# Performance work log

Measured on AMD Instinct MI355X. Metric: run time of the kernel, lower is better.

Reference implementation:

```python
import jax, jax.numpy as jnp
import numpy as np

DIM, N_HEAD, N_KV, HEAD_DIM = 4096, 32, 8, 128
B, S = 2, 2048


def apply_rotary_emb(x, freqs_cis):
    # x: [B, S, H, D]; freqs_cis: [S, D//2, 2]
    xs = x.reshape(x.shape[:-1] + (-1, 2))            # [B,S,H,D/2,2]
    f = freqs_cis.reshape(1, xs.shape[1], 1, xs.shape[3], 2)
    x0, x1 = xs[..., 0], xs[..., 1]
    f0, f1 = f[..., 0], f[..., 1]
    out = jnp.stack([x0 * f0 - x1 * f1, x0 * f1 + x1 * f0], axis=-1)
    return out.reshape(x.shape).astype(x.dtype)


def setup_inputs() -> dict:
    key = jax.random.key(0)
    k1, k2, k3, k4 = jax.random.split(key, 4)
    x = jax.random.normal(k1, (B, S, DIM), dtype=jnp.float32)
    freqs_cis = jax.random.normal(k2, (S, HEAD_DIM // 2, 2), dtype=jnp.float32)
    # causal boolean mask (True = attend)
    mask_cache = jnp.tril(jnp.ones((S, S), dtype=bool))[None, None]
    input_pos = jnp.arange(S, dtype=jnp.int32)
    total_head_dim = (N_HEAD + 2 * N_KV) * HEAD_DIM
    wqkv = jax.random.normal(k3, (total_head_dim, DIM), dtype=jnp.float32) * (DIM ** -0.5)
    wo = jax.random.normal(k4, (DIM, DIM), dtype=jnp.float32) * (DIM ** -0.5)
    return {"x": x, "freqs_cis": freqs_cis, "mask_cache": mask_cache,
            "input_pos": input_pos, "wqkv": wqkv, "wo": wo}


def reference(x, freqs_cis, mask_cache, input_pos, wqkv, wo):
    bsz, seqlen, _ = x.shape
    kv_size = N_KV * HEAD_DIM
    qkv = jnp.einsum('bsd,fd->bsf', x, wqkv)
    q, k, v = jnp.split(qkv, [DIM, DIM + kv_size], axis=-1)
    q = q.reshape(bsz, seqlen, N_HEAD, HEAD_DIM)
    k = k.reshape(bsz, seqlen, N_KV, HEAD_DIM)
    v = v.reshape(bsz, seqlen, N_KV, HEAD_DIM)
    q = apply_rotary_emb(q, freqs_cis)
    k = apply_rotary_emb(k, freqs_cis)
    q = q.transpose(0, 2, 1, 3)   # [B,Hq,S,D]
    k = k.transpose(0, 2, 1, 3)   # [B,Hkv,S,D]
    v = v.transpose(0, 2, 1, 3)
    # GQA: repeat kv heads to match query heads
    g = N_HEAD // N_KV
    k = jnp.repeat(k, g, axis=1)
    v = jnp.repeat(v, g, axis=1)
    scale = 1.0 / jnp.sqrt(jnp.asarray(HEAD_DIM, dtype=q.dtype))
    scores = jnp.einsum('bhqd,bhkd->bhqk', q, k) * scale
    neg_inf = jnp.asarray(jnp.finfo(scores.dtype).min, dtype=scores.dtype)
    scores = jnp.where(mask_cache, scores, neg_inf)
    attn = jax.nn.softmax(scores, axis=-1)
    y = jnp.einsum('bhqk,bhkd->bhqd', attn, v)
    y = y.transpose(0, 2, 1, 3).reshape(bsz, seqlen, DIM)
    return jnp.einsum('bsd,od->bso', y, wo)
```

## Files before the change

### kernel.cpp

```cpp
#include <hip/hip_runtime.h>
#include <hip/hip_bf16.h>

#define DIM   4096
#define NHEAD 32
#define NKV   8
#define HD    128
#define BATCH 2
#define SEQ   2048
#define M1    (BATCH*SEQ)
#define NF    ((NHEAD+2*NKV)*HD)

typedef __attribute__((ext_vector_type(8))) short short8;
typedef __attribute__((ext_vector_type(4))) short short4v;
typedef __attribute__((ext_vector_type(4))) float f32x4;

__device__ __forceinline__ float bf2f(short s) {
    unsigned u = ((unsigned)(unsigned short)s) << 16;
    return __builtin_bit_cast(float, u);
}
__device__ __forceinline__ short f2bf(float f) {
    unsigned u = __builtin_bit_cast(unsigned, f);
    u = u + 0x7fffu + ((u >> 16) & 1u);
    return (short)(u >> 16);
}

__device__ __forceinline__ void gload_lds16(const void* g, void* l) {
    __builtin_amdgcn_global_load_lds(
        (const __attribute__((address_space(1))) void*)g,
        (__attribute__((address_space(3))) void*)l, 16, 0, 0);
}

__global__ void f2bf2_k(const float* __restrict__ a, short* __restrict__ da, int na8,
                        const float* __restrict__ b, short* __restrict__ db, int nb8) {
    const int total = na8 + nb8;
    const int stride = gridDim.x * blockDim.x;
    for (int i = blockIdx.x * blockDim.x + threadIdx.x; i < total; i += stride) {
        const float* s; short* d; int j = i;
        if (j < na8) { s = a; d = da; }
        else         { j -= na8; s = b; d = db; }
        float4 v0 = ((const float4*)s)[2*j];
        float4 v1 = ((const float4*)s)[2*j + 1];
        short8 o;
        o[0] = f2bf(v0.x); o[1] = f2bf(v0.y); o[2] = f2bf(v0.z); o[3] = f2bf(v0.w);
        o[4] = f2bf(v1.x); o[5] = f2bf(v1.y); o[6] = f2bf(v1.z); o[7] = f2bf(v1.w);
        ((short8*)d)[j] = o;
    }
}
__global__ void f2bf_k(const float* __restrict__ src, short* __restrict__ dst, int n8) {
    const int stride = gridDim.x * blockDim.x;
    for (int i = blockIdx.x * blockDim.x + threadIdx.x; i < n8; i += stride) {
        float4 v0 = ((const float4*)src)[2*i];
        float4 v1 = ((const float4*)src)[2*i + 1];
        short8 o;
        o[0] = f2bf(v0.x); o[1] = f2bf(v0.y); o[2] = f2bf(v0.z); o[3] = f2bf(v0.w);
        o[4] = f2bf(v1.x); o[5] = f2bf(v1.y); o[6] = f2bf(v1.z); o[7] = f2bf(v1.w);
        ((short8*)dst)[i] = o;
    }
}

template<int OUT_BF16>
__global__ __launch_bounds__(512, 2) void gemm256(const short* __restrict__ A,
                                                  const short* __restrict__ Bm,
                                                  void* __restrict__ Cout,
                                                  int M, int N, int K) {
    __shared__ __align__(16) short As[2][2][128*64];
    __shared__ __align__(16) short Bs[2][2][128*64];
    const int nbn = N >> 8;
    const int nwg = gridDim.x;
    const int cpx = nwg >> 3;
    const int swz = (blockIdx.x & 7) * cpx + (blockIdx.x >> 3);
    const int brow = swz / nbn, bcol = swz % nbn;
    const int t = threadIdx.x, lane = t & 63, w = t >> 6;
    const int wm = w >> 2, wn = w & 3;
    const int l16 = lane & 15, lhi = lane >> 4, l7 = l16 & 7;
    const size_t abase = (size_t)brow * 256 * K;
    const size_t bbase = (size_t)bcol * 256 * K;
    const int sr = t >> 3;
    const int sc = t & 7;
    const int scl = sc ^ (sr & 7);
    f32x4 acc[8][4] = {};

    auto stageA = [&](int kt, int qm) {
#pragma unroll
        for (int i = 0; i < 2; ++i)
            gload_lds16(A + abase + (size_t)(i*128 + qm*64 + sr) * K + kt*64 + scl*8,
                        &As[kt & 1][qm][(i*64 + sr)*64 + sc*8]);
    };
    auto stageB = [&](int kt, int qn) {
#pragma unroll
        for (int i = 0; i < 2; ++i)
            gload_lds16(Bm + bbase + (size_t)((i*2 + (sr>>5))*64 + qn*32 + (sr & 31)) * K + kt*64 + scl*8,
                        &Bs[kt & 1][qn][(i*64 + sr)*64 + sc*8]);
    };

    const int NT = K >> 6;
    stageA(0, 0); stageB(0, 0); stageA(0, 1); stageB(0, 1);
    stageA(1, 0); stageB(1, 0);
    asm volatile("s_waitcnt vmcnt(4)" ::: "memory");
    __builtin_amdgcn_s_barrier();

    short8 a0[4][2], a1[4][2], b0[2][2], b1[2][2];

#define LD_A(dst, P, QM)                                                        \
    _Pragma("unroll") for (int mi = 0; mi < 4; ++mi)                            \
    _Pragma("unroll") for (int kk = 0; kk < 2; ++kk)                            \
        dst[mi][kk] = *(const short8*)&As[P][QM][(wm*64 + mi*16 + l16)*64 + (((kk*4 + lhi) ^ l7) * 8)];
#define LD_B(dst, P, QN)                                                        \
    _Pragma("unroll") for (int ni = 0; ni < 2; ++ni)                            \
    _Pragma("unroll") for (int kk = 0; kk < 2; ++kk)                            \
        dst[ni][kk] = *(const short8*)&Bs[P][QN][(wn*32 + ni*16 + l16)*64 + (((kk*4 + lhi) ^ l7) * 8)];
#define MMA(QM, QN, af, bf)                                                     \
    __builtin_amdgcn_s_barrier();                                               \
    __builtin_amdgcn_s_setprio(1);                                              \
    _Pragma("unroll") for (int kk = 0; kk < 2; ++kk)                            \
    _Pragma("unroll") for (int mi = 0; mi < 4; ++mi)                            \
    _Pragma("unroll") for (int ni = 0; ni < 2; ++ni)                            \
        acc[QM*4 + mi][QN*2 + ni] = __builtin_amdgcn_mfma_f32_16x16x32_bf16(    \
            af[mi][kk], bf[ni][kk], acc[QM*4 + mi][QN*2 + ni], 0, 0, 0);        \
    __builtin_amdgcn_s_setprio(0);

    LD_A(a0, 0, 0)
    LD_B(b0, 0, 0)

    for (int cur = 0; cur < NT; ++cur) {
        const int d = cur & 1, dn = d ^ 1;
        LD_B(b1, d, 1)
        if (cur + 1 < NT) stageA(cur + 1, 1);
        MMA(0, 0, a0, b0)
        asm volatile("s_waitcnt vmcnt(2)" ::: "memory");
        LD_A(a1, d, 1)
        if (cur + 1 < NT) stageB(cur + 1, 1);
        MMA(0, 1, a0, b1)
        LD_A(a0, dn, 0)
        if (cur + 2 < NT) stageA(cur + 2, 0);
        MMA(1, 0, a1, b0)
        if (cur + 2 < NT) { asm volatile("s_waitcnt vmcnt(2)" ::: "memory"); }
        else              { asm volatile("s_waitcnt vmcnt(0)" ::: "memory"); }
        LD_B(b0, dn, 0)
        if (cur + 2 < NT) stageB(cur + 2, 0);
        MMA(1, 1, a1, b1)
    }
#undef LD_A
#undef LD_B
#undef MMA

#pragma unroll
    for (int fm = 0; fm < 8; ++fm)
#pragma unroll
        for (int fn = 0; fn < 4; ++fn)
#pragma unroll
            for (int r = 0; r < 4; ++r) {
                size_t row = (size_t)brow*256 + wm*128 + fm*16 + lhi*4 + r;
                size_t col = (size_t)bcol*256 + wn*64 + fn*16 + l16;
                if (OUT_BF16)
                    ((short*)Cout)[row * N + col] = f2bf(acc[fm][fn][r]);
                else
                    ((float*)Cout)[row * N + col] = acc[fm][fn][r];
            }
}

#define ROPE_BLKS (M1*640/256)
__global__ __launch_bounds__(256) void prep_k(const short* __restrict__ qkv,
                                              const float* __restrict__ freqs,
                                              short* __restrict__ qb,
                                              short* __restrict__ kb,
                                              short* __restrict__ vg) {
    __shared__ short Ls[32][130];
    const int t = threadIdx.x;
    if (blockIdx.x < ROPE_BLKS) {
        int tid  = blockIdx.x * 256 + t;
        int colg = tid % 640;
        int row  = tid / 640;
        int b = row >> 11, s = row & 2047;
        int f = colg << 3;
        int h = f >> 7, d = f & 127;
        short8 v = *(const short8*)&qkv[(size_t)row * NF + f];
        const float4 fa = *(const float4*)&freqs[(size_t)(s*64 + (d>>1)) * 2];
        const float4 fb = *(const float4*)&freqs[(size_t)(s*64 + (d>>1)) * 2 + 4];
        float fr[8] = {fa.x, fa.y, fa.z, fa.w, fb.x, fb.y, fb.z, fb.w};
        short8 o;
#pragma unroll
        for (int p = 0; p < 4; ++p) {
            float x0 = bf2f(v[2*p]), x1 = bf2f(v[2*p+1]);
            float c = fr[2*p], sn = fr[2*p+1];
            o[2*p]   = f2bf(x0 * c  - x1 * sn);
            o[2*p+1] = f2bf(x0 * sn + x1 * c);
        }
        if (h < NHEAD)
            *(short8*)&qb[((((size_t)b*NHEAD + h)*SEQ + s) << 7) + d] = o;
        else
            *(short8*)&kb[((((size_t)b*NKV + (h - NHEAD))*SEQ + s) << 7) + d] = o;
    } else {
        const int bid = blockIdx.x - ROPE_BLKS;
        const int st = bid & 63, kv = (bid >> 6) & 7, b = bid >> 9;
        const int dcol = (t & 15) * 8, sl = t >> 4;
#pragma unroll
        for (int p = 0; p < 2; ++p) {
            int s = p*16 + sl;
            short8 v = *(const short8*)&qkv[(size_t)(b*2048 + st*32 + s)*NF + 5120 + kv*128 + dcol];
#pragma unroll
            for (int j = 0; j < 8; ++j) Ls[s][dcol + j] = v[j];
        }
        __syncthreads();
        size_t base = (((size_t)b*NKV + kv) << 18) + st*4096;
#pragma unroll
        for (int p = 0; p < 2; ++p) {
            int c = p*256 + t;
            short8 o;
#pragma unroll
            for (int j = 0; j < 8; ++j) o[j] = Ls[(c & 3)*8 + j][c >> 2];
            *(short8*)&vg[base + c*8] = o;
        }
    }
}

__global__ __launch_bounds__(256, 3) void attn_k(const short* __restrict__ qb_,
                                                 const short* __restrict__ kb_,
                                                 const short* __restrict__ vg_,
                                                 short* __restrict__ yb) {
    __shared__ __align__(16) short Ks[2][32*128];
    __shared__ __align__(16) short Vs[2][128*32];
    __shared__ __align__(16) short Pw[4][32*36];
    const int bid = blockIdx.x;
    const int qt = 15 - (bid >> 6);
    const int bh = bid & 63;
    const int b = bh >> 5, h = bh & 31, kv = h >> 2;
    const int t = threadIdx.x, lane = t & 63, w = t >> 6;
    const int l16 = lane & 15, lhi = lane >> 4;
    const short* Qp = qb_ + (((size_t)(b*NHEAD + h)*SEQ + qt*128 + w*32) << 7);
    const short* Kp = kb_ + (((size_t)(b*NKV + kv)*SEQ) << 7);
    const short* Vp = vg_ + (((size_t)(b*NKV + kv)*SEQ) << 7);
    short8 qf[2][4];
#pragma unroll
    for (int qq = 0; qq < 2; ++qq)
#pragma unroll
        for (int kk = 0; kk < 4; ++kk)
            qf[qq][kk] = *(const short8*)&Qp[(qq*16 + l16)*HD + kk*32 + lhi*8];
    f32x4 oacc[2][8] = {};
    float mrow[2] = {-1e30f, -1e30f};
    float lsum[2] = {0.f, 0.f};
    const int NT = (qt + 1) * 4;
    const int qmaxw = qt*128 + w*32 + 31;
    const float sc = 0.08838834764831845f;

    auto stage = [&](int kt, int buf) {
#pragma unroll
        for (int i = 0; i < 2; ++i) {
            int L = i*256 + t;
            int r = L >> 4, s = L & 15;
            int gs = (s & 8) | ((s & 7) ^ (r & 7));
            gload_lds16(Kp + (size_t)kt*4096 + r*128 + gs*8, &Ks[buf][L*8]);
        }
#pragma unroll
        for (int i = 0; i < 2; ++i) {
            int L = i*256 + t;
            int r8 = L >> 3, s3 = L & 7;
            int gs = s3 ^ (r8 & 7);
            gload_lds16(Vp + (size_t)kt*4096 + (r8*8 + gs)*8, &Vs[buf][L*8]);
        }
    };

    stage(0, 0);
    __syncthreads();
    int cur = 0;
    for (int kt = 0; kt < NT; ++kt) {
        if (kt + 1 < NT) stage(kt + 1, cur ^ 1);
        if (kt*32 <= qmaxw) {
            f32x4 sT[2][2] = {};
#pragma unroll
            for (int kk = 0; kk < 4; ++kk) {
                short8 kf[2];
#pragma unroll
                for (int kb2 = 0; kb2 < 2; ++kb2) {
                    int row = kb2*16 + l16;
                    int ch  = kk*4 + lhi;
                    int chs = (ch & 8) | ((ch & 7) ^ (row & 7));
                    kf[kb2] = *(const short8*)&Ks[cur][row*128 + chs*8];
                }
#pragma unroll
                for (int kb2 = 0; kb2 < 2; ++kb2)
#pragma unroll
                    for (int qq = 0; qq < 2; ++qq)
                        sT[kb2][qq] = __builtin_amdgcn_mfma_f32_16x16x32_bf16(kf[kb2], qf[qq][kk], sT[kb2][qq], 0, 0, 0);
            }
#pragma unroll
            for (int qq = 0; qq < 2; ++qq) {
                int qg = qt*128 + w*32 + qq*16 + l16;
                float tmax = -1e30f;
#pragma unroll
                for (int kb2 = 0; kb2 < 2; ++kb2)
#pragma unroll
                    for (int r = 0; r < 4; ++r) {
                        int kg = kt*32 + kb2*16 + lhi*4 + r;
                        float sv = sT[kb2][qq][r] * sc;
                        sv = (kg > qg) ? -1e30f : sv;
                        sT[kb2][qq][r] = sv;
                        tmax = fmaxf(tmax, sv);
                    }
                tmax = fmaxf(tmax, __shfl_xor(tmax, 16, 64));
                tmax = fmaxf(tmax, __shfl_xor(tmax, 32, 64));
                float mn;
                bool noresc = __all(tmax <= mrow[qq] + 8.0f);
                if (noresc) { mn = mrow[qq]; }
                else        { mn = fmaxf(mrow[qq], tmax); }
                float rsum = 0.f;
#pragma unroll
                for (int kb2 = 0; kb2 < 2; ++kb2) {
                    short4v pk;
#pragma unroll
                    for (int r = 0; r < 4; ++r) {
                        float p = __expf(sT[kb2][qq][r] - mn);
                        rsum += p;
                        pk[r] = f2bf(p);
                    }
                    *(short4v*)&Pw[w][(qq*16 + l16)*36 + kb2*16 + lhi*4] = pk;
                }
                rsum += __shfl_xor(rsum, 16, 64);
                rsum += __shfl_xor(rsum, 32, 64);
                if (noresc) {
                    lsum[qq] += rsum;
                } else {
                    float alpha = __expf(mrow[qq] - mn);
                    mrow[qq] = mn;
                    lsum[qq] = lsum[qq]*alpha + rsum;
                    float a4[4];
#pragma unroll
                    for (int r = 0; r < 4; ++r)
                        a4[r] = __shfl(alpha, (lane & 48) | (lhi*4 + r), 64);
#pragma unroll
                    for (int n = 0; n < 8; ++n)
#pragma unroll
                        for (int r = 0; r < 4; ++r)
                            oacc[qq][n][r] *= a4[r];
                }
            }
            short8 pf[2];
#pragma unroll
            for (int qq = 0; qq < 2; ++qq)
                pf[qq] = *(const short8*)&Pw[w][(qq*16 + l16)*36 + lhi*8];
#pragma unroll
            for (int n = 0; n < 8; ++n) {
                int d   = n*16 + l16;
                int lch = d*4 + lhi;
                int phys = (lch & ~7) | ((lch & 7) ^ ((lch >> 3) & 7));
                short8 vf = *(const short8*)&Vs[cur][phys*8];
#pragma unroll
                for (int qq = 0; qq < 2; ++qq)
                    oacc[qq][n] = __builtin_amdgcn_mfma_f32_16x16x32_bf16(pf[qq], vf, oacc[qq][n], 0, 0, 0);
            }
        }
        __syncthreads();
        cur ^= 1;
    }
#pragma unroll
    for (int qq = 0; qq < 2; ++qq) {
        float inv = 1.f / lsum[qq];
        float i4[4];
#pragma unroll
        for (int r = 0; r < 4; ++r)
            i4[r] = __shfl(inv, (lane & 48) | (lhi*4 + r), 64);
#pragma unroll
        for (int n = 0; n < 8; ++n)
#pragma unroll
            for (int r = 0; r < 4; ++r) {
                size_t row = (size_t)b*SEQ + qt*128 + w*32 + qq*16 + lhi*4 + r;
                yb[row*DIM + h*HD + n*16 + l16] = f2bf(oacc[qq][n][r] * i4[r]);
            }
    }
}

extern "C" void kernel_launch(void* const* d_in, const int* in_sizes, int n_in,
                              void* d_out, int out_size, void* d_ws, size_t ws_size,
                              hipStream_t stream) {
    const float* x     = (const float*)d_in[0];
    const float* freqs = (const float*)d_in[1];
    const float* wqkv  = (const float*)d_in[4];
    const float* wo    = (const float*)d_in[5];
    float* out = (float*)d_out;
    char* ws = (char*)d_ws;
    const size_t MB = 1024*1024;
    short* xb    = (short*)ws;
    short* yb    = (short*)ws;
    short* wqkvb = (short*)(ws + 32*MB);
    short* wob   = (short*)(ws + 32*MB);
    short* qkvb  = (short*)(ws + 80*MB);
    short* qb    = (short*)(ws + 128*MB);
    short* kb    = (short*)(ws + 160*MB);
    short* vg    = (short*)(ws + 168*MB);

    const int na8 = DIM*DIM/8, nb8 = NF*DIM/8;
    f2bf2_k<<<2048, 256, 0, stream>>>(x, xb, na8, wqkv, wqkvb, nb8);
    gemm256<1><<<(M1/256)*(NF/256), 512, 0, stream>>>(xb, wqkvb, qkvb, M1, NF, DIM);
    prep_k<<<ROPE_BLKS + BATCH*NKV*(SEQ/32), 256, 0, stream>>>(qkvb, freqs, qb, kb, vg);
    attn_k<<<BATCH*NHEAD*(SEQ/128), 256, 0, stream>>>(qb, kb, vg, yb);
    f2bf_k<<<2048, 256, 0, stream>>>(wo, wob, DIM*DIM/8);
    gemm256<0><<<(M1/256)*(DIM/256), 512, 0, stream>>>(yb, wob, out, M1, DIM, DIM);
}
```

Before: 504.6 us.

## Split-K the tail tiles of the QKV GEMM to fix wave quantization

The QKV GEMM has 384 tiles of 256x256. The first 256 tiles now run as full-K blocks, and the remaining 128 tiles are split in two along K across 256 blocks, so the launch has 512 blocks and fills the CUs more evenly. Split blocks atomically add fp32 partials into a zeroed scratch slab. The second block to finish, detected through a per-tile counter, converts the slab to bf16. This adds a memset of about 32MB, atomic traffic and an extra pass over the slab in exchange for better load balance.

```diff
diff --git a/kernel.cpp b/kernel.cpp
--- a/kernel.cpp
+++ b/kernel.cpp
@@ -58,48 +58,54 @@
     }
 }
 
-template<int OUT_BF16>
-__global__ __launch_bounds__(512, 2) void gemm256(const short* __restrict__ A,
-                                                  const short* __restrict__ Bm,
-                                                  void* __restrict__ Cout,
-                                                  int M, int N, int K) {
-    __shared__ __align__(16) short As[2][2][128*64];
-    __shared__ __align__(16) short Bs[2][2][128*64];
-    const int nbn = N >> 8;
-    const int nwg = gridDim.x;
-    const int cpx = nwg >> 3;
-    const int swz = (blockIdx.x & 7) * cpx + (blockIdx.x >> 3);
-    const int brow = swz / nbn, bcol = swz % nbn;
-    const int t = threadIdx.x, lane = t & 63, w = t >> 6;
-    const int wm = w >> 2, wn = w & 3;
-    const int l16 = lane & 15, lhi = lane >> 4, l7 = l16 & 7;
-    const size_t abase = (size_t)brow * 256 * K;
-    const size_t bbase = (size_t)bcol * 256 * K;
-    const int sr = t >> 3;
-    const int sc = t & 7;
-    const int scl = sc ^ (sr & 7);
-    f32x4 acc[8][4] = {};
-
-    auto stageA = [&](int kt, int qm) {
-#pragma unroll
-        for (int i = 0; i < 2; ++i)
-            gload_lds16(A + abase + (size_t)(i*128 + qm*64 + sr) * K + kt*64 + scl*8,
-                        &As[kt & 1][qm][(i*64 + sr)*64 + sc*8]);
-    };
-    auto stageB = [&](int kt, int qn) {
-#pragma unroll
-        for (int i = 0; i < 2; ++i)
-            gload_lds16(Bm + bbase + (size_t)((i*2 + (sr>>5))*64 + qn*32 + (sr & 31)) * K + kt*64 + scl*8,
-                        &Bs[kt & 1][qn][(i*64 + sr)*64 + sc*8]);
-    };
-
-    const int NT = K >> 6;
-    stageA(0, 0); stageB(0, 0); stageA(0, 1); stageB(0, 1);
-    stageA(1, 0); stageB(1, 0);
-    asm volatile("s_waitcnt vmcnt(4)" ::: "memory");
-    __builtin_amdgcn_s_barrier();
-
-    short8 a0[4][2], a1[4][2], b0[2][2], b1[2][2];
+#define GEMM_CORE(NTv, KB6, EPILOG)                                             \
+    const int t = threadIdx.x, lane = t & 63, w = t >> 6;                       \
+    const int wm = w >> 2, wn = w & 3;                                          \
+    const int l16 = lane & 15, lhi = lane >> 4, l7 = l16 & 7;                   \
+    const size_t abase = (size_t)brow * 256 * K;                                \
+    const size_t bbase = (size_t)bcol * 256 * K;                                \
+    const int sr = t >> 3;                                                      \
+    const int sc = t & 7;                                                       \
+    const int scl = sc ^ (sr & 7);                                              \
+    f32x4 acc[8][4] = {};                                                       \
+    auto stageA = [&](int kt, int qm) {                                         \
+        _Pragma("unroll") for (int i = 0; i < 2; ++i)                           \
+            gload_lds16(A + abase + (size_t)(i*128 + qm*64 + sr) * K + kt*64 + scl*8, \
+                        &As[kt & 1][qm][(i*64 + sr)*64 + sc*8]);                \
+    };                                                                          \
+    auto stageB = [&](int kt, int qn) {                                         \
+        _Pragma("unroll") for (int i = 0; i < 2; ++i)                           \
+            gload_lds16(Bm + bbase + (size_t)((i*2 + (sr>>5))*64 + qn*32 + (sr & 31)) * K + kt*64 + scl*8, \
+                        &Bs[kt & 1][qn][(i*64 + sr)*64 + sc*8]);                \
+    };                                                                          \
+    const int NT = (NTv);                                                       \
+    const int kb6 = (KB6);                                                      \
+    stageA(kb6, 0); stageB(kb6, 0); stageA(kb6, 1); stageB(kb6, 1);             \
+    stageA(kb6 + 1, 0); stageB(kb6 + 1, 0);                                     \
+    asm volatile("s_waitcnt vmcnt(4)" ::: "memory");                            \
+    __builtin_amdgcn_s_barrier();                                               \
+    short8 a0[4][2], a1[4][2], b0[2][2], b1[2][2];                              \
+    LD_A(a0, 0, 0)                                                              \
+    LD_B(b0, 0, 0)                                                              \
+    for (int cur = 0; cur < NT; ++cur) {                                        \
+        const int d = cur & 1, dn = d ^ 1;                                      \
+        LD_B(b1, d, 1)                                                          \
+        if (cur + 1 < NT) stageA(kb6 + cur + 1, 1);                             \
+        MMA(0, 0, a0, b0)                                                       \
+        asm volatile("s_waitcnt vmcnt(2)" ::: "memory");                        \
+        LD_A(a1, d, 1)                                                          \
+        if (cur + 1 < NT) stageB(kb6 + cur + 1, 1);                             \
+        MMA(0, 1, a0, b1)                                                       \
+        LD_A(a0, dn, 0)                                                         \
+        if (cur + 2 < NT) stageA(kb6 + cur + 2, 0);                             \
+        MMA(1, 0, a1, b0)                                                       \
+        if (cur + 2 < NT) { asm volatile("s_waitcnt vmcnt(2)" ::: "memory"); }  \
+        else              { asm volatile("s_waitcnt vmcnt(0)" ::: "memory"); }  \
+        LD_B(b0, dn, 0)                                                         \
+        if (cur + 2 < NT) stageB(kb6 + cur + 2, 0);                             \
+        MMA(1, 1, a1, b1)                                                       \
+    }                                                                           \
+    EPILOG
 
 #define LD_A(dst, P, QM)                                                        \
     _Pragma("unroll") for (int mi = 0; mi < 4; ++mi)                            \
@@ -119,44 +125,89 @@
             af[mi][kk], bf[ni][kk], acc[QM*4 + mi][QN*2 + ni], 0, 0, 0);        \
     __builtin_amdgcn_s_setprio(0);
 
-    LD_A(a0, 0, 0)
-    LD_B(b0, 0, 0)
-
-    for (int cur = 0; cur < NT; ++cur) {
-        const int d = cur & 1, dn = d ^ 1;
-        LD_B(b1, d, 1)
-        if (cur + 1 < NT) stageA(cur + 1, 1);
-        MMA(0, 0, a0, b0)
-        asm volatile("s_waitcnt vmcnt(2)" ::: "memory");
-        LD_A(a1, d, 1)
-        if (cur + 1 < NT) stageB(cur + 1, 1);
-        MMA(0, 1, a0, b1)
-        LD_A(a0, dn, 0)
-        if (cur + 2 < NT) stageA(cur + 2, 0);
-        MMA(1, 0, a1, b0)
-        if (cur + 2 < NT) { asm volatile("s_waitcnt vmcnt(2)" ::: "memory"); }
-        else              { asm volatile("s_waitcnt vmcnt(0)" ::: "memory"); }
-        LD_B(b0, dn, 0)
-        if (cur + 2 < NT) stageB(cur + 2, 0);
-        MMA(1, 1, a1, b1)
-    }
-#undef LD_A
-#undef LD_B
-#undef MMA
-
-#pragma unroll
-    for (int fm = 0; fm < 8; ++fm)
-#pragma unroll
-        for (int fn = 0; fn < 4; ++fn)
-#pragma unroll
-            for (int r = 0; r < 4; ++r) {
+template<int OUT_BF16>
+__global__ __launch_bounds__(512, 2) void gemm256(const short* __restrict__ A,
+                                                  const short* __restrict__ Bm,
+                                                  void* __restrict__ Cout,
+                                                  int M, int N, int K) {
+    __shared__ __align__(16) short As[2][2][128*64];
+    __shared__ __align__(16) short Bs[2][2][128*64];
+    const int nbn = N >> 8;
+    const int nwg = gridDim.x;
+    const int cpx = nwg >> 3;
+    const int swz = (blockIdx.x & 7) * cpx + (blockIdx.x >> 3);
+    const int brow = swz / nbn, bcol = swz % nbn;
+    GEMM_CORE(K >> 6, 0,
+        _Pragma("unroll") for (int fm = 0; fm < 8; ++fm)
+        _Pragma("unroll") for (int fn = 0; fn < 4; ++fn)
+        _Pragma("unroll") for (int r = 0; r < 4; ++r) {
+            size_t row = (size_t)brow*256 + wm*128 + fm*16 + lhi*4 + r;
+            size_t col = (size_t)bcol*256 + wn*64 + fn*16 + l16;
+            if (OUT_BF16) ((short*)Cout)[row * N + col] = f2bf(acc[fm][fn][r]);
+            else          ((float*)Cout)[row * N + col] = acc[fm][fn][r];
+        })
+}
+
+__global__ __launch_bounds__(512, 2) void gemm_qkv(const short* __restrict__ A,
+                                                   const short* __restrict__ Bm,
+                                                   short* __restrict__ Cout,
+                                                   float* __restrict__ part,
+                                                   unsigned* __restrict__ flag) {
+    __shared__ __align__(16) short As[2][2][128*64];
+    __shared__ __align__(16) short Bs[2][2][128*64];
+    __shared__ unsigned oldf;
+    const int K = DIM;
+    const int bid = blockIdx.x;
+    int brow, bcol, ntv, kb, p = 0;
+    bool split;
+    if (bid < 256) {
+        int swz = (bid & 7) * 32 + (bid >> 3);
+        brow = swz / 24; bcol = swz % 24;
+        ntv = 64; kb = 0; split = false;
+    } else {
+        int i = bid - 256;
+        p = i >> 1;
+        int h = i & 1;
+        int ps = (p & 7) * 16 + (p >> 3);
+        int tile = 256 + ps;
+        brow = tile / 24; bcol = tile % 24;
+        ntv = 32; kb = h * 32; split = true;
+    }
+    GEMM_CORE(ntv, kb,
+        if (!split) {
+            _Pragma("unroll") for (int fm = 0; fm < 8; ++fm)
+            _Pragma("unroll") for (int fn = 0; fn < 4; ++fn)
+            _Pragma("unroll") for (int r = 0; r < 4; ++r) {
                 size_t row = (size_t)brow*256 + wm*128 + fm*16 + lhi*4 + r;
                 size_t col = (size_t)bcol*256 + wn*64 + fn*16 + l16;
-                if (OUT_BF16)
-                    ((short*)Cout)[row * N + col] = f2bf(acc[fm][fn][r]);
-                else
-                    ((float*)Cout)[row * N + col] = acc[fm][fn][r];
-            }
+                Cout[row * NF + col] = f2bf(acc[fm][fn][r]);
+            }
+        } else {
+            float* slab = part + (size_t)p * 65536;
+            _Pragma("unroll") for (int fm = 0; fm < 8; ++fm)
+            _Pragma("unroll") for (int fn = 0; fn < 4; ++fn)
+            _Pragma("unroll") for (int r = 0; r < 4; ++r) {
+                int lrow = wm*128 + fm*16 + lhi*4 + r;
+                int lcol = wn*64 + fn*16 + l16;
+                atomicAdd(&slab[lrow*256 + lcol], acc[fm][fn][r]);
+            }
+            __threadfence();
+            __syncthreads();
+            if (t == 0) oldf = atomicAdd(flag + p, 1u);
+            __syncthreads();
+            if (oldf == 1) {
+                __threadfence();
+                _Pragma("unroll") for (int fm = 0; fm < 8; ++fm)
+                _Pragma("unroll") for (int fn = 0; fn < 4; ++fn)
+                _Pragma("unroll") for (int r = 0; r < 4; ++r) {
+                    int lrow = wm*128 + fm*16 + lhi*4 + r;
+                    int lcol = wn*64 + fn*16 + l16;
+                    size_t row = (size_t)brow*256 + lrow;
+                    size_t col = (size_t)bcol*256 + lcol;
+                    Cout[row * NF + col] = f2bf(slab[lrow*256 + lcol]);
+                }
+            }
+        })
 }
 
 #define ROPE_BLKS (M1*640/256)
@@ -385,12 +436,15 @@
     short* wob   = (short*)(ws + 32*MB);
     short* qkvb  = (short*)(ws + 80*MB);
     short* qb    = (short*)(ws + 128*MB);
+    float* part  = (float*)(ws + 128*MB);
+    unsigned* flg = (unsigned*)(ws + 160*MB);
     short* kb    = (short*)(ws + 160*MB);
     short* vg    = (short*)(ws + 168*MB);
 
     const int na8 = DIM*DIM/8, nb8 = NF*DIM/8;
+    hipMemsetAsync(ws + 128*MB, 0, 32*MB + 512, stream);
     f2bf2_k<<<2048, 256, 0, stream>>>(x, xb, na8, wqkv, wqkvb, nb8);
-    gemm256<1><<<(M1/256)*(NF/256), 512, 0, stream>>>(xb, wqkvb, qkvb, M1, NF, DIM);
+    gemm_qkv<<<512, 512, 0, stream>>>(xb, wqkvb, qkvb, part, flg);
     prep_k<<<ROPE_BLKS + BATCH*NKV*(SEQ/32), 256, 0, stream>>>(qkvb, freqs, qb, kb, vg);
     attn_k<<<BATCH*NHEAD*(SEQ/128), 256, 0, stream>>>(qb, kb, vg, yb);
     f2bf_k<<<2048, 256, 0, stream>>>(wo, wob, DIM*DIM/8);
```

After: 604.7 us. +19.8%, slower.
